# Kernel tuning notes

Measured on AMD Instinct MI355X. Metric: run time of the kernel, lower is better.

The kernel has to match this reference:

```python
import jax, jax.numpy as jnp
import numpy as np

SR = 44100
D = SR * 30          # duration_samples = 1_323_000
N = 1024             # number of note events
L = 32768            # max note length in samples
W = 1024             # hann window length (module's window_length)
H = 8                # harmonics in the synth
K = 128              # FIR taps in the effect chain
LAT = 2              # time_latent_size


def setup_inputs() -> dict:
    key = jax.random.key(0)
    ks = jax.random.split(key, 10)
    freq_rad = jax.random.uniform(ks[0], (N,), jnp.float32, 0.01, 0.3)
    velocity = jax.random.uniform(ks[1], (N,), jnp.float32, 1.0, 127.0)
    starts = jax.random.randint(ks[2], (N,), 0, D - L, dtype=jnp.int32)
    lengths = jax.random.randint(ks[3], (N,), 2048, L + 1, dtype=jnp.int32)
    # time_embedder: Linear(1,32) -> ReLU -> Linear(32,LAT)
    w1 = jax.random.normal(ks[4], (1, 32), jnp.float32)
    b1 = jnp.zeros((32,), jnp.float32)
    w2 = jax.random.normal(ks[5], (32, LAT), jnp.float32) / jnp.sqrt(32.0)
    b2 = jnp.zeros((LAT,), jnp.float32)
    # synth amplitude MLP: [freq, vel, latent] (2+LAT) -> 64 -> H
    ws1 = jax.random.normal(ks[6], (2 + LAT, 64), jnp.float32)
    bs1 = jnp.zeros((64,), jnp.float32)
    ws2 = jax.random.normal(ks[7], (64, H), jnp.float32) / 8.0
    bs2 = jnp.zeros((H,), jnp.float32)
    # effect chain: causal FIR (OIW layout) + tanh
    fir = jax.random.normal(ks[8], (1, 1, K), jnp.float32) / K
    return dict(freq_rad=freq_rad, velocity=velocity,
                w1=w1, b1=b1, w2=w2, b2=b2,
                ws1=ws1, bs1=bs1, ws2=ws2, bs2=bs2, fir=fir,
                starts=starts, lengths=lengths, duration_samples=D)


def reference(freq_rad, velocity, w1, b1, w2, b2, ws1, bs1, ws2, bs2, fir,
              starts, lengths, duration_samples):
    Dn = int(duration_samples)
    t = jnp.arange(L, dtype=jnp.float32)            # [L]
    ti = jnp.arange(L, dtype=jnp.int32)             # [L]
    ends = starts + lengths
    # output_length = min(end, duration) - start, clipped to [0, L]
    out_len = jnp.clip(jnp.minimum(ends, Dn) - starts, 0, L)  # [N]
    # time latent: MLP on normalized start time
    nt = (starts.astype(jnp.float32) / Dn)[:, None]           # [N,1]
    lat = jax.nn.relu(nt @ w1 + b1) @ w2 + b2                  # [N,LAT]
    vel = (velocity / 127.0)[:, None]                          # [N,1]
    # harmonic amplitudes from tiny MLP (the 'synth')
    feat = jnp.concatenate([freq_rad[:, None], vel, lat], axis=-1)  # [N,2+LAT]
    amps = jax.nn.softplus(jax.nn.relu(feat @ ws1 + bs1) @ ws2 + bs2)  # [N,H]
    # additive synthesis; fixed small loop over harmonics, vectorized over [N,L]
    phase = freq_rad[:, None] * t[None, :]                     # [N,L]
    seg = jnp.zeros((N, L), jnp.float32)
    for hh in range(1, H + 1):
        seg = seg + amps[:, hh - 1:hh] * jnp.sin(hh * phase)
    seg = seg * vel
    # hann window (torch periodic) on the LAST W samples of each variable-length segment
    n = jnp.arange(W, dtype=jnp.float32)
    hann = 0.5 * (1.0 - jnp.cos(2.0 * jnp.pi * n / W))         # [W]
    wpos = ti[None, :] - (out_len[:, None] - W)                # [N,L]
    in_win = (wpos >= 0) & (wpos < W)
    factor = jnp.where(in_win, hann[jnp.clip(wpos, 0, W - 1)], 1.0)
    mask = (ti[None, :] < out_len[:, None]).astype(jnp.float32)  # zero past segment end
    seg = seg * factor * mask
    # effect chain: causal 128-tap FIR then tanh (masked so padding stays silent)
    y = jax.lax.conv_general_dilated(seg[:, None, :], fir,
                                     window_strides=(1,), padding=[(K - 1, 0)])
    seg = jnp.tanh(y[:, 0, :]) * mask                          # [N,L]
    # overlap-add: scatter each note into the output buffer
    idx = starts[:, None] + ti[None, :]                        # [N,L]
    valid = (ti[None, :] < out_len[:, None]) & (idx < Dn)
    contrib = jnp.where(valid, seg, 0.0)
    out = jnp.zeros((Dn,), jnp.float32).at[jnp.clip(idx, 0, Dn - 1).reshape(-1)].add(
        contrib.reshape(-1))
    return out
```

## Files before the change

kernel.cpp:

```cpp
#include <hip/hip_runtime.h>
#include <math.h>

#define LMAX  32768
#define WWIN  1024
#define KFIR  128
#define WOUT  512
#define TO    1024
#define CPAD  656
#define NMAX  1024
#define PMAX  96

typedef _Float16 v8h __attribute__((ext_vector_type(8)));
typedef _Float16 v4h __attribute__((ext_vector_type(4)));
typedef float    v4f __attribute__((ext_vector_type(4)));

__device__ __forceinline__ float fast_tanh(float x) {
    float e = __builtin_amdgcn_exp2f(x * 2.8853900817779268f);
    return fmaf(-2.0f, __builtin_amdgcn_rcpf(e + 1.0f), 1.0f);
}

__global__ __launch_bounds__(256, 3) void synth_fused_k(
    const float* __restrict__ freq_g, const float* __restrict__ velo_g,
    const float* __restrict__ w1,  const float* __restrict__ b1,
    const float* __restrict__ w2,  const float* __restrict__ b2,
    const float* __restrict__ ws1, const float* __restrict__ bs1,
    const float* __restrict__ ws2, const float* __restrict__ bs2,
    const float* __restrict__ fir,
    const int* __restrict__ starts, const int* __restrict__ lengths,
    float* __restrict__ out, int Dn, int N)
{
    __shared__ __align__(16) _Float16 segc[4][4][CPAD];
    __shared__ float fir_s[KFIR];
    __shared__ unsigned short note_list[NMAX];
    __shared__ int note_cnt;
    __shared__ float s_w1[32], s_b1[32], s_w2[64], s_b2[2];
    __shared__ float s_ws1[256], s_bs1[64], s_ws2[512], s_bs2[8];
    __shared__ int   stl[PMAX], oll[PMAX];
    __shared__ float fl[PMAX];
    __shared__ __align__(16) float ampsl[PMAX][8];

    const int tid  = threadIdx.x;
    const int wid  = tid >> 6;
    const int lane = tid & 63;
    const int m    = lane & 15;
    const int quad = lane >> 4;
    const int grp  = wid >> 1;
    const int o0   = blockIdx.x * TO;
    const int o_end = min(o0 + TO, Dn);
    const int ow   = o0 + (wid & 1) * WOUT;

    if (tid < 128) fir_s[tid] = fir[tid];
    if (tid < 32) { s_w1[tid] = w1[tid]; s_b1[tid] = b1[tid]; }
    if (tid < 64) { s_w2[tid] = w2[tid]; s_bs1[tid] = bs1[tid]; }
    if (tid < 2)  s_b2[tid] = b2[tid];
    if (tid < 8)  s_bs2[tid] = bs2[tid];
    s_ws1[tid] = ws1[tid];
    s_ws2[tid] = ws2[tid];  s_ws2[tid + 256] = ws2[tid + 256];
    if (tid == 0) note_cnt = 0;
    __syncthreads();

    for (int j = tid; j < N; j += 256) {
        int st = starts[j];
        int len = lengths[j];
        int ol = min(st + len, Dn) - st;
        ol = max(0, min(ol, LMAX));
        if (st < o_end && st + ol > o0) {
            int p = atomicAdd(&note_cnt, 1);
            note_list[p] = (unsigned short)j;
        }
    }
    __syncthreads();
    const int K = note_cnt;

    const int kn0 = min(K, PMAX);
    if (tid < kn0) {
        const int nid = (int)note_list[tid];
        int st  = starts[nid];
        int len = lengths[nid];
        int ol  = min(st + len, Dn) - st;
        ol = max(0, min(ol, LMAX));
        stl[tid] = st;
        oll[tid] = ol;
        float v = velo_g[nid] * (1.0f / 127.0f);
        float f = freq_g[nid];
        fl[tid] = f;
        float nt = (float)st / (float)Dn;
        float lat0 = s_b2[0], lat1 = s_b2[1];
        #pragma unroll
        for (int j = 0; j < 32; ++j) {
            float h = fmaxf(fmaf(nt, s_w1[j], s_b1[j]), 0.0f);
            lat0 = fmaf(h, s_w2[j * 2 + 0], lat0);
            lat1 = fmaf(h, s_w2[j * 2 + 1], lat1);
        }
        float acc[8];
        #pragma unroll
        for (int h = 0; h < 8; ++h) acc[h] = s_bs2[h];
        #pragma unroll
        for (int j = 0; j < 64; ++j) {
            float a = s_bs1[j];
            a = fmaf(f,    s_ws1[0 * 64 + j], a);
            a = fmaf(v,    s_ws1[1 * 64 + j], a);
            a = fmaf(lat0, s_ws1[2 * 64 + j], a);
            a = fmaf(lat1, s_ws1[3 * 64 + j], a);
            a = fmaxf(a, 0.0f);
            #pragma unroll
            for (int h = 0; h < 8; ++h)
                acc[h] = fmaf(a, s_ws2[j * 8 + h], acc[h]);
        }
        #pragma unroll
        for (int h = 0; h < 8; ++h) {
            float a = acc[h];
            float sp = fmaxf(a, 0.0f) + log1pf(expf(-fabsf(a)));
            ampsl[tid][h] = sp * v;
        }
    }

    v8h afrag[12];
    #pragma unroll
    for (int t = 0; t < 12; ++t) {
        v8h af;
        #pragma unroll
        for (int j = 0; j < 8; ++j) {
            int idx = 32 * t + 8 * quad + j - 16 * m;
            float fv = (idx >= 0 && idx < KFIR) ? fir_s[idx] : 0.0f;
            af[j] = (_Float16)fv;
        }
        afrag[t] = af;
    }
    for (int z = lane; z < 4 * 20; z += 64) {
        int S = z / 20, off = z % 20;
        segc[wid][S][636 + off] = (_Float16)0.0f;
    }
    __syncthreads();

    const _Float16* __restrict__ bbase = &segc[wid][m & 3][(m & ~3) + 8 * quad];

    float accA0 = 0.f, accA1 = 0.f, accA2 = 0.f, accA3 = 0.f;
    float accB0 = 0.f, accB1 = 0.f, accB2 = 0.f, accB3 = 0.f;

    const double inv2pi = 0.15915494309189535;

    for (int c = 0; c < K; c += PMAX) {
        const int kn = min(K - c, PMAX);

        if (c > 0) {
            __syncthreads();
            if (tid < kn) {
                const int nid = (int)note_list[c + tid];
                int st  = starts[nid];
                int len = lengths[nid];
                int ol  = min(st + len, Dn) - st;
                ol = max(0, min(ol, LMAX));
                stl[tid] = st;
                oll[tid] = ol;
                float v = velo_g[nid] * (1.0f / 127.0f);
                float f = freq_g[nid];
                fl[tid] = f;
                float nt = (float)st / (float)Dn;
                float lat0 = s_b2[0], lat1 = s_b2[1];
                #pragma unroll
                for (int j = 0; j < 32; ++j) {
                    float h = fmaxf(fmaf(nt, s_w1[j], s_b1[j]), 0.0f);
                    lat0 = fmaf(h, s_w2[j * 2 + 0], lat0);
                    lat1 = fmaf(h, s_w2[j * 2 + 1], lat1);
                }
                float acc[8];
                #pragma unroll
                for (int h = 0; h < 8; ++h) acc[h] = s_bs2[h];
                #pragma unroll
                for (int j = 0; j < 64; ++j) {
                    float a = s_bs1[j];
                    a = fmaf(f,    s_ws1[0 * 64 + j], a);
                    a = fmaf(v,    s_ws1[1 * 64 + j], a);
                    a = fmaf(lat0, s_ws1[2 * 64 + j], a);
                    a = fmaf(lat1, s_ws1[3 * 64 + j], a);
                    a = fmaxf(a, 0.0f);
                    #pragma unroll
                    for (int h = 0; h < 8; ++h)
                        acc[h] = fmaf(a, s_ws2[j * 8 + h], acc[h]);
                }
                #pragma unroll
                for (int h = 0; h < 8; ++h) {
                    float a = acc[h];
                    float sp = fmaxf(a, 0.0f) + log1pf(expf(-fabsf(a)));
                    ampsl[tid][h] = sp * v;
                }
            }
            __syncthreads();
        }

        int stN = 0, olN = 0; float fN = 0.f;
        float4 amN0 = {}, amN1 = {};
        if (grp < kn) {
            stN = stl[grp]; olN = oll[grp]; fN = fl[grp];
            amN0 = *(const float4*)&ampsl[grp][0];
            amN1 = *(const float4*)&ampsl[grp][4];
        }

        for (int kk = grp; kk < kn; kk += 2) {
            const int st = stN, ol = olN;
            const float f = fN;
            const float4 am0 = amN0, am1 = amN1;
            if (kk + 2 < kn) {
                stN = stl[kk + 2]; olN = oll[kk + 2]; fN = fl[kk + 2];
                amN0 = *(const float4*)&ampsl[kk + 2][0];
                amN1 = *(const float4*)&ampsl[kk + 2][4];
            }

            const int base = ow - st;
            if (base >= ol || base + WOUT <= 0) continue;

            const float A0 = am0.x, A1 = am0.y, A2 = am0.z, A3 = am0.w;
            const float A4 = am1.x, A5 = am1.y, A6 = am1.z, A7 = am1.w;
            const double fd = (double)f;

            const int tseed = base - 127 + lane;
            double rev0 = fd * (double)tseed * inv2pi;
            float r0 = (float)(rev0 - floor(rev0));
            float s = __builtin_amdgcn_sinf(r0);
            float cc = __builtin_amdgcn_cosf(r0);
            double d64 = fd * 64.0 * inv2pi;
            float r64 = (float)(d64 - floor(d64));
            const float sd = __builtin_amdgcn_sinf(r64);
            const float cd = __builtin_amdgcn_cosf(r64);
            const int wbase = ol - WWIN;

            const bool interior = (base >= 127) && (base + 513 <= wbase);

            if (interior) {
                #pragma unroll
                for (int i = 0; i < 10; ++i) {
                    float tc = cc + cc;
                    float sA = s;
                    float sum = A0 * sA;
                    float sB = tc * sA;              sum = fmaf(A1, sB, sum);
                    float sC = fmaf(tc, sB, -sA);    sum = fmaf(A2, sC, sum);
                    float sD = fmaf(tc, sC, -sB);    sum = fmaf(A3, sD, sum);
                    float sE = fmaf(tc, sD, -sC);    sum = fmaf(A4, sE, sum);
                    float sF = fmaf(tc, sE, -sD);    sum = fmaf(A5, sF, sum);
                    float sG = fmaf(tc, sF, -sE);    sum = fmaf(A6, sG, sum);
                    float sH = fmaf(tc, sG, -sF);    sum = fmaf(A7, sH, sum);
                    _Float16 h = (_Float16)sum;
                    const int x = lane + 64 * i;
                    if (i == 0) {
                        #pragma unroll
                        for (int S = 0; S < 4; ++S)
                            if (x >= S) segc[wid][S][x - S] = h;
                    } else {
                        #pragma unroll
                        for (int S = 0; S < 4; ++S)
                            segc[wid][S][x - S] = h;
                    }
                    float ns = fmaf(s, cd, cc * sd);
                    float nc = fmaf(cc, cd, -(s * sd));
                    s = ns; cc = nc;
                }
            } else {
                #pragma unroll
                for (int i = 0; i < 10; ++i) {
                    int t = tseed + 64 * i;
                    float val = 0.0f;
                    if (t >= 0 && t < ol) {
                        float tc = cc + cc;
                        float sA = s;
                        float sum = A0 * sA;
                        float sB = tc * sA;              sum = fmaf(A1, sB, sum);
                        float sC = fmaf(tc, sB, -sA);    sum = fmaf(A2, sC, sum);
                        float sD = fmaf(tc, sC, -sB);    sum = fmaf(A3, sD, sum);
                        float sE = fmaf(tc, sD, -sC);    sum = fmaf(A4, sE, sum);
                        float sF = fmaf(tc, sE, -sD);    sum = fmaf(A5, sF, sum);
                        float sG = fmaf(tc, sF, -sE);    sum = fmaf(A6, sG, sum);
                        float sH = fmaf(tc, sG, -sF);    sum = fmaf(A7, sH, sum);
                        int wpos = t - wbase;
                        float factor = 1.0f;
                        if (wpos >= 0)
                            factor = 0.5f - 0.5f * __builtin_amdgcn_cosf((float)wpos * (1.0f / WWIN));
                        val = sum * factor;
                    }
                    _Float16 h = (_Float16)val;
                    const int x = lane + 64 * i;
                    if (i == 0) {
                        #pragma unroll
                        for (int S = 0; S < 4; ++S)
                            if (x >= S) segc[wid][S][x - S] = h;
                    } else {
                        #pragma unroll
                        for (int S = 0; S < 4; ++S)
                            segc[wid][S][x - S] = h;
                    }
                    float ns = fmaf(s, cd, cc * sd);
                    float nc = fmaf(cc, cd, -(s * sd));
                    s = ns; cc = nc;
                }
            }

            v4f CA0 = {0.f, 0.f, 0.f, 0.f};
            v4f CA1 = {0.f, 0.f, 0.f, 0.f};
            v4f CB0 = {0.f, 0.f, 0.f, 0.f};
            v4f CB1 = {0.f, 0.f, 0.f, 0.f};
            #pragma unroll
            for (int t = 0; t < 6; ++t) {
                v4h lo = *(const v4h*)(bbase + 32 * t);
                v4h hi = *(const v4h*)(bbase + 32 * t + 4);
                v8h bf = __builtin_shufflevector(lo, hi, 0, 1, 2, 3, 4, 5, 6, 7);
                CA0 = __builtin_amdgcn_mfma_f32_16x16x32_f16(afrag[t], bf, CA0, 0, 0, 0);
                v4h lo2 = *(const v4h*)(bbase + 256 + 32 * t);
                v4h hi2 = *(const v4h*)(bbase + 256 + 32 * t + 4);
                v8h bf2 = __builtin_shufflevector(lo2, hi2, 0, 1, 2, 3, 4, 5, 6, 7);
                CB0 = __builtin_amdgcn_mfma_f32_16x16x32_f16(afrag[t], bf2, CB0, 0, 0, 0);
            }
            #pragma unroll
            for (int t = 6; t < 12; ++t) {
                v4h lo = *(const v4h*)(bbase + 32 * t);
                v4h hi = *(const v4h*)(bbase + 32 * t + 4);
                v8h bf = __builtin_shufflevector(lo, hi, 0, 1, 2, 3, 4, 5, 6, 7);
                CA1 = __builtin_amdgcn_mfma_f32_16x16x32_f16(afrag[t], bf, CA1, 0, 0, 0);
                v4h lo2 = *(const v4h*)(bbase + 256 + 32 * t);
                v4h hi2 = *(const v4h*)(bbase + 256 + 32 * t + 4);
                v8h bf2 = __builtin_shufflevector(lo2, hi2, 0, 1, 2, 3, 4, 5, 6, 7);
                CB1 = __builtin_amdgcn_mfma_f32_16x16x32_f16(afrag[t], bf2, CB1, 0, 0, 0);
            }

            {
                const int tb = base + 64 * quad + m;
                float y;
                y = CA0[0] + CA1[0]; if (tb +   0 >= 0 && tb +   0 < ol) accA0 += fast_tanh(y);
                y = CA0[1] + CA1[1]; if (tb +  16 >= 0 && tb +  16 < ol) accA1 += fast_tanh(y);
                y = CA0[2] + CA1[2]; if (tb +  32 >= 0 && tb +  32 < ol) accA2 += fast_tanh(y);
                y = CA0[3] + CA1[3]; if (tb +  48 >= 0 && tb +  48 < ol) accA3 += fast_tanh(y);
                y = CB0[0] + CB1[0]; if (tb + 256 >= 0 && tb + 256 < ol) accB0 += fast_tanh(y);
                y = CB0[1] + CB1[1]; if (tb + 272 >= 0 && tb + 272 < ol) accB1 += fast_tanh(y);
                y = CB0[2] + CB1[2]; if (tb + 288 >= 0 && tb + 288 < ol) accB2 += fast_tanh(y);
                y = CB0[3] + CB1[3]; if (tb + 304 >= 0 && tb + 304 < ol) accB3 += fast_tanh(y);
            }
        }
    }

    __syncthreads();
    float* red = (float*)&segc[0][0][0];
    const int rb = (wid & 1) * WOUT + 64 * quad + m;
    if (grp == 1) {
        red[rb +   0] = accA0;
        red[rb +  16] = accA1;
        red[rb +  32] = accA2;
        red[rb +  48] = accA3;
        red[rb + 256] = accB0;
        red[rb + 272] = accB1;
        red[rb + 288] = accB2;
        red[rb + 304] = accB3;
    }
    __syncthreads();
    if (grp == 0) {
        const int ob = o0 + rb;
        if (ob +   0 < Dn) out[ob +   0] = accA0 + red[rb +   0];
        if (ob +  16 < Dn) out[ob +  16] = accA1 + red[rb +  16];
        if (ob +  32 < Dn) out[ob +  32] = accA2 + red[rb +  32];
        if (ob +  48 < Dn) out[ob +  48] = accA3 + red[rb +  48];
        if (ob + 256 < Dn) out[ob + 256] = accB0 + red[rb + 256];
        if (ob + 272 < Dn) out[ob + 272] = accB1 + red[rb + 272];
        if (ob + 288 < Dn) out[ob + 288] = accB2 + red[rb + 288];
        if (ob + 304 < Dn) out[ob + 304] = accB3 + red[rb + 304];
    }
}

extern "C" void kernel_launch(void* const* d_in, const int* in_sizes, int n_in,
                              void* d_out, int out_size, void* d_ws, size_t ws_size,
                              hipStream_t stream) {
    const float* freq    = (const float*)d_in[0];
    const float* velo    = (const float*)d_in[1];
    const float* w1      = (const float*)d_in[2];
    const float* b1      = (const float*)d_in[3];
    const float* w2      = (const float*)d_in[4];
    const float* b2      = (const float*)d_in[5];
    const float* ws1     = (const float*)d_in[6];
    const float* bs1     = (const float*)d_in[7];
    const float* ws2     = (const float*)d_in[8];
    const float* bs2     = (const float*)d_in[9];
    const float* fir     = (const float*)d_in[10];
    const int*   starts  = (const int*)d_in[11];
    const int*   lengths = (const int*)d_in[12];

    const int N  = in_sizes[0];
    const int Dn = out_size;
    float* out = (float*)d_out;

    int n_tiles = (Dn + TO - 1) / TO;
    synth_fused_k<<<n_tiles, 256, 0, stream>>>(
        freq, velo, w1, b1, w2, b2, ws1, bs1, ws2, bs2,
        fir, starts, lengths, out, Dn, N);
}
```

Before: 143.8 us.

## Assign each wave a full 1024-sample window and split notes across four waves

Each wave now covers the whole 1024-sample output tile instead of half of it, and notes are spread across four waves rather than two. This halves the redundant 127-sample FIR halo synthesis per note (1152 synthesized samples per 1024 outputs instead of 640 per 512) and the per-note setup cost. The trade-offs are doubled accumulator registers and a larger shared-memory staging buffer, which may reduce occupancy under the 3-block launch bound. The final reduction now sums partials from four waves instead of two.

```diff
diff --git a/kernel.cpp b/kernel.cpp
--- a/kernel.cpp
+++ b/kernel.cpp
@@ -4,9 +4,11 @@
 #define LMAX  32768
 #define WWIN  1024
 #define KFIR  128
-#define WOUT  512
+#define WOUT  1024
 #define TO    1024
-#define CPAD  656
+#define CPAD  1232
+#define SYNTH 1152
+#define ZPS   1148
 #define NMAX  1024
 #define PMAX  96
 
@@ -44,10 +46,10 @@
     const int lane = tid & 63;
     const int m    = lane & 15;
     const int quad = lane >> 4;
-    const int grp  = wid >> 1;
+    const int grp  = wid;
     const int o0   = blockIdx.x * TO;
     const int o_end = min(o0 + TO, Dn);
-    const int ow   = o0 + (wid & 1) * WOUT;
+    const int ow   = o0;
 
     if (tid < 128) fir_s[tid] = fir[tid];
     if (tid < 32) { s_w1[tid] = w1[tid]; s_b1[tid] = b1[tid]; }
@@ -127,16 +129,17 @@
         }
         afrag[t] = af;
     }
-    for (int z = lane; z < 4 * 20; z += 64) {
-        int S = z / 20, off = z % 20;
-        segc[wid][S][636 + off] = (_Float16)0.0f;
+    for (int z = lane; z < 4 * (CPAD - ZPS); z += 64) {
+        int S = z / (CPAD - ZPS), off = z % (CPAD - ZPS);
+        segc[wid][S][ZPS + off] = (_Float16)0.0f;
     }
     __syncthreads();
 
     const _Float16* __restrict__ bbase = &segc[wid][m & 3][(m & ~3) + 8 * quad];
 
-    float accA0 = 0.f, accA1 = 0.f, accA2 = 0.f, accA3 = 0.f;
-    float accB0 = 0.f, accB1 = 0.f, accB2 = 0.f, accB3 = 0.f;
+    float accv[16];
+    #pragma unroll
+    for (int r = 0; r < 16; ++r) accv[r] = 0.0f;
 
     const double inv2pi = 0.15915494309189535;
 
@@ -197,14 +200,14 @@
             amN1 = *(const float4*)&ampsl[grp][4];
         }
 
-        for (int kk = grp; kk < kn; kk += 2) {
+        for (int kk = grp; kk < kn; kk += 4) {
             const int st = stN, ol = olN;
             const float f = fN;
             const float4 am0 = amN0, am1 = amN1;
-            if (kk + 2 < kn) {
-                stN = stl[kk + 2]; olN = oll[kk + 2]; fN = fl[kk + 2];
-                amN0 = *(const float4*)&ampsl[kk + 2][0];
-                amN1 = *(const float4*)&ampsl[kk + 2][4];
+            if (kk + 4 < kn) {
+                stN = stl[kk + 4]; olN = oll[kk + 4]; fN = fl[kk + 4];
+                amN0 = *(const float4*)&ampsl[kk + 4][0];
+                amN1 = *(const float4*)&ampsl[kk + 4][4];
             }
 
             const int base = ow - st;
@@ -225,11 +228,11 @@
             const float cd = __builtin_amdgcn_cosf(r64);
             const int wbase = ol - WWIN;
 
-            const bool interior = (base >= 127) && (base + 513 <= wbase);
+            const bool interior = (base >= 127) && (base + WOUT + 1 <= wbase);
 
             if (interior) {
                 #pragma unroll
-                for (int i = 0; i < 10; ++i) {
+                for (int i = 0; i < SYNTH / 64; ++i) {
                     float tc = cc + cc;
                     float sA = s;
                     float sum = A0 * sA;
@@ -257,7 +260,7 @@
                 }
             } else {
                 #pragma unroll
-                for (int i = 0; i < 10; ++i) {
+                for (int i = 0; i < SYNTH / 64; ++i) {
                     int t = tseed + 64 * i;
                     float val = 0.0f;
                     if (t >= 0 && t < ol) {
@@ -294,72 +297,76 @@
                 }
             }
 
-            v4f CA0 = {0.f, 0.f, 0.f, 0.f};
-            v4f CA1 = {0.f, 0.f, 0.f, 0.f};
-            v4f CB0 = {0.f, 0.f, 0.f, 0.f};
-            v4f CB1 = {0.f, 0.f, 0.f, 0.f};
             #pragma unroll
-            for (int t = 0; t < 6; ++t) {
-                v4h lo = *(const v4h*)(bbase + 32 * t);
-                v4h hi = *(const v4h*)(bbase + 32 * t + 4);
-                v8h bf = __builtin_shufflevector(lo, hi, 0, 1, 2, 3, 4, 5, 6, 7);
-                CA0 = __builtin_amdgcn_mfma_f32_16x16x32_f16(afrag[t], bf, CA0, 0, 0, 0);
-                v4h lo2 = *(const v4h*)(bbase + 256 + 32 * t);
-                v4h hi2 = *(const v4h*)(bbase + 256 + 32 * t + 4);
-                v8h bf2 = __builtin_shufflevector(lo2, hi2, 0, 1, 2, 3, 4, 5, 6, 7);
-                CB0 = __builtin_amdgcn_mfma_f32_16x16x32_f16(afrag[t], bf2, CB0, 0, 0, 0);
-            }
+            for (int p = 0; p < 2; ++p) {
+                const int co = 512 * p;
+                v4f CA0 = {0.f, 0.f, 0.f, 0.f};
+                v4f CA1 = {0.f, 0.f, 0.f, 0.f};
+                v4f CB0 = {0.f, 0.f, 0.f, 0.f};
+                v4f CB1 = {0.f, 0.f, 0.f, 0.f};
+                #pragma unroll
+                for (int t = 0; t < 6; ++t) {
+                    v4h lo = *(const v4h*)(bbase + co + 32 * t);
+                    v4h hi = *(const v4h*)(bbase + co + 32 * t + 4);
+                    v8h bf = __builtin_shufflevector(lo, hi, 0, 1, 2, 3, 4, 5, 6, 7);
+                    CA0 = __builtin_amdgcn_mfma_f32_16x16x32_f16(afrag[t], bf, CA0, 0, 0, 0);
+                    v4h lo2 = *(const v4h*)(bbase + co + 256 + 32 * t);
+                    v4h hi2 = *(const v4h*)(bbase + co + 256 + 32 * t + 4);
+                    v8h bf2 = __builtin_shufflevector(lo2, hi2, 0, 1, 2, 3, 4, 5, 6, 7);
+                    CB0 = __builtin_amdgcn_mfma_f32_16x16x32_f16(afrag[t], bf2, CB0, 0, 0, 0);
+                }
+                #pragma unroll
+                for (int t = 6; t < 12; ++t) {
+                    v4h lo = *(const v4h*)(bbase + co + 32 * t);
+                    v4h hi = *(const v4h*)(bbase + co + 32 * t + 4);
+                    v8h bf = __builtin_shufflevector(lo, hi, 0, 1, 2, 3, 4, 5, 6, 7);
+                    CA1 = __builtin_amdgcn_mfma_f32_16x16x32_f16(afrag[t], bf, CA1, 0, 0, 0);
+                    v4h lo2 = *(const v4h*)(bbase + co + 256 + 32 * t);
+                    v4h hi2 = *(const v4h*)(bbase + co + 256 + 32 * t + 4);
+                    v8h bf2 = __builtin_shufflevector(lo2, hi2, 0, 1, 2, 3, 4, 5, 6, 7);
+                    CB1 = __builtin_amdgcn_mfma_f32_16x16x32_f16(afrag[t], bf2, CB1, 0, 0, 0);
+                }
+
+                const int tb = base + co + 64 * quad + m;
+                float y;
+                y = CA0[0] + CA1[0]; if (tb +   0 >= 0 && tb +   0 < ol) accv[p*8+0] += fast_tanh(y);
+                y = CA0[1] + CA1[1]; if (tb +  16 >= 0 && tb +  16 < ol) accv[p*8+1] += fast_tanh(y);
+                y = CA0[2] + CA1[2]; if (tb +  32 >= 0 && tb +  32 < ol) accv[p*8+2] += fast_tanh(y);
+                y = CA0[3] + CA1[3]; if (tb +  48 >= 0 && tb +  48 < ol) accv[p*8+3] += fast_tanh(y);
+                y = CB0[0] + CB1[0]; if (tb + 256 >= 0 && tb + 256 < ol) accv[p*8+4] += fast_tanh(y);
+                y = CB0[1] + CB1[1]; if (tb + 272 >= 0 && tb + 272 < ol) accv[p*8+5] += fast_tanh(y);
+                y = CB0[2] + CB1[2]; if (tb + 288 >= 0 && tb + 288 < ol) accv[p*8+6] += fast_tanh(y);
+                y = CB0[3] + CB1[3]; if (tb + 304 >= 0 && tb + 304 < ol) accv[p*8+7] += fast_tanh(y);
+            }
+        }
+    }
+
+    __syncthreads();
+    float* red = (float*)&segc[0][0][0];
+    const int slot0 = 64 * quad + m;
+    if (grp != 0) {
+        float* rg = red + (grp - 1) * 1024;
+        #pragma unroll
+        for (int p = 0; p < 2; ++p) {
             #pragma unroll
-            for (int t = 6; t < 12; ++t) {
-                v4h lo = *(const v4h*)(bbase + 32 * t);
-                v4h hi = *(const v4h*)(bbase + 32 * t + 4);
-                v8h bf = __builtin_shufflevector(lo, hi, 0, 1, 2, 3, 4, 5, 6, 7);
-                CA1 = __builtin_amdgcn_mfma_f32_16x16x32_f16(afrag[t], bf, CA1, 0, 0, 0);
-                v4h lo2 = *(const v4h*)(bbase + 256 + 32 * t);
-                v4h hi2 = *(const v4h*)(bbase + 256 + 32 * t + 4);
-                v8h bf2 = __builtin_shufflevector(lo2, hi2, 0, 1, 2, 3, 4, 5, 6, 7);
-                CB1 = __builtin_amdgcn_mfma_f32_16x16x32_f16(afrag[t], bf2, CB1, 0, 0, 0);
-            }
-
-            {
-                const int tb = base + 64 * quad + m;
-                float y;
-                y = CA0[0] + CA1[0]; if (tb +   0 >= 0 && tb +   0 < ol) accA0 += fast_tanh(y);
-                y = CA0[1] + CA1[1]; if (tb +  16 >= 0 && tb +  16 < ol) accA1 += fast_tanh(y);
-                y = CA0[2] + CA1[2]; if (tb +  32 >= 0 && tb +  32 < ol) accA2 += fast_tanh(y);
-                y = CA0[3] + CA1[3]; if (tb +  48 >= 0 && tb +  48 < ol) accA3 += fast_tanh(y);
-                y = CB0[0] + CB1[0]; if (tb + 256 >= 0 && tb + 256 < ol) accB0 += fast_tanh(y);
-                y = CB0[1] + CB1[1]; if (tb + 272 >= 0 && tb + 272 < ol) accB1 += fast_tanh(y);
-                y = CB0[2] + CB1[2]; if (tb + 288 >= 0 && tb + 288 < ol) accB2 += fast_tanh(y);
-                y = CB0[3] + CB1[3]; if (tb + 304 >= 0 && tb + 304 < ol) accB3 += fast_tanh(y);
-            }
-        }
-    }
-
-    __syncthreads();
-    float* red = (float*)&segc[0][0][0];
-    const int rb = (wid & 1) * WOUT + 64 * quad + m;
-    if (grp == 1) {
-        red[rb +   0] = accA0;
-        red[rb +  16] = accA1;
-        red[rb +  32] = accA2;
-        red[rb +  48] = accA3;
-        red[rb + 256] = accB0;
-        red[rb + 272] = accB1;
-        red[rb + 288] = accB2;
-        red[rb + 304] = accB3;
+            for (int r = 0; r < 8; ++r) {
+                const int idx = slot0 + 512 * p + (r >> 2) * 256 + (r & 3) * 16;
+                rg[idx] = accv[p * 8 + r];
+            }
+        }
     }
     __syncthreads();
     if (grp == 0) {
-        const int ob = o0 + rb;
-        if (ob +   0 < Dn) out[ob +   0] = accA0 + red[rb +   0];
-        if (ob +  16 < Dn) out[ob +  16] = accA1 + red[rb +  16];
-        if (ob +  32 < Dn) out[ob +  32] = accA2 + red[rb +  32];
-        if (ob +  48 < Dn) out[ob +  48] = accA3 + red[rb +  48];
-        if (ob + 256 < Dn) out[ob + 256] = accB0 + red[rb + 256];
-        if (ob + 272 < Dn) out[ob + 272] = accB1 + red[rb + 272];
-        if (ob + 288 < Dn) out[ob + 288] = accB2 + red[rb + 288];
-        if (ob + 304 < Dn) out[ob + 304] = accB3 + red[rb + 304];
+        #pragma unroll
+        for (int p = 0; p < 2; ++p) {
+            #pragma unroll
+            for (int r = 0; r < 8; ++r) {
+                const int idx = slot0 + 512 * p + (r >> 2) * 256 + (r & 3) * 16;
+                float v = accv[p * 8 + r] + red[idx] + red[1024 + idx] + red[2048 + idx];
+                const int ob = o0 + idx;
+                if (ob < Dn) out[ob] = v;
+            }
+        }
     }
 }
 
```

Measured after the change: 143.5 us. Within noise of the previous version (-0.2%).
